# Kernel tuning notes

Hardware: AMD Instinct MI355X
Metric: run time of the kernel (lower is better)

The kernel has to match this reference:

```python
import jax, jax.numpy as jnp
import numpy as np

B, S, D, H = 2, 2048, 1024, 16
DK = D // H


def setup_inputs() -> dict:
    key = jax.random.key(0)
    ks = jax.random.split(key, 9)
    def xavier(k, shape):
        fan_in, fan_out = shape[1], shape[0]
        lim = jnp.sqrt(6.0 / (fan_in + fan_out))
        return jax.random.uniform(k, shape, jnp.float32, -lim, lim)
    x = jax.random.normal(ks[0], (B, S, D), jnp.float32)
    mask = jnp.ones((B, 1, S), jnp.int32)
    Wq = xavier(ks[1], (D, D)); bq = jnp.zeros((D,), jnp.float32)
    Wk = xavier(ks[2], (D, D)); bk = jnp.zeros((D,), jnp.float32)
    Wv = xavier(ks[3], (D, D)); bv = jnp.zeros((D,), jnp.float32)
    Wo = xavier(ks[4], (D, D)); bo = jnp.zeros((D,), jnp.float32)
    return {"x": x, "mask": mask, "Wq": Wq, "bq": bq, "Wk": Wk, "bk": bk,
            "Wv": Wv, "bv": bv, "Wo": Wo, "bo": bo}


def reference(x, mask, Wq, bq, Wk, bk, Wv, bv, Wo, bo):
    # Linear layers use torch convention y = x @ W.T + b
    q = (x @ Wq.T + bq).reshape(B, S, H, DK).transpose(0, 2, 1, 3)  # [B,H,S,DK]
    k = (x @ Wk.T + bk).reshape(B, S, H, DK).transpose(0, 2, 1, 3)
    v = (x @ Wv.T + bv).reshape(B, S, H, DK).transpose(0, 2, 1, 3)
    scores = jnp.einsum('bhqd,bhkd->bhqk', q, k) / jnp.sqrt(jnp.float32(DK))
    m = mask[:, None, :, :]  # unsqueeze(1): broadcast over heads -> [B,1,1,S]
    scores = jnp.where(m == 0, jnp.float32(-1e9), scores)
    p = jax.nn.softmax(scores, axis=-1)  # dropout p=0.0 -> identity
    ctx = jnp.einsum('bhqk,bhkd->bhqd', p, v)
    ctx = ctx.transpose(0, 2, 1, 3).reshape(B, S, D)
    return ctx @ Wo.T + bo
```

## Files before the change

### kernel.cpp

```cpp
#include <hip/hip_runtime.h>
#include <hip/hip_bf16.h>
#include <math.h>

#define Bn 2
#define Sn 2048
#define Dn 1024
#define Hn 16
#define DKn 64
#define BHS (Bn * Hn * Sn)

using fragb  = __attribute__((ext_vector_type(8))) short;
using frag16 = __attribute__((ext_vector_type(8))) _Float16;
using f4     = __attribute__((ext_vector_type(4))) float;

__device__ __forceinline__ short f2bf(float f) {
    union { float f; unsigned u; } v; v.f = f;
    unsigned r = v.u + 0x7FFF + ((v.u >> 16) & 1);
    return (short)(r >> 16);
}
__device__ __forceinline__ short f2h(float f) {
    _Float16 h = (_Float16)f;
    short s; __builtin_memcpy(&s, &h, 2); return s;
}

#define GLOAD(gptr, lptr)                                                     \
    __builtin_amdgcn_global_load_lds(                                         \
        (const __attribute__((address_space(1))) unsigned int*)(const void*)(gptr), \
        (__attribute__((address_space(3))) unsigned int*)(void*)(lptr), 16, 0, 0)

#define NX (Bn * Sn * Dn)
#define NW (Dn * Dn)

__global__ __launch_bounds__(256) void prep(
    const float* __restrict__ x,  const float* __restrict__ Wq,
    const float* __restrict__ Wk, const float* __restrict__ Wv,
    const float* __restrict__ Wo, const int* __restrict__ mask,
    short* __restrict__ xh,
    short* __restrict__ Wqh, short* __restrict__ Wkh,
    short* __restrict__ Wvh, short* __restrict__ Woh,
    short* __restrict__ mfb)
{
    int i = blockIdx.x * 256 + threadIdx.x;
    const float* src; short* dst; int j;
    if (i < NX)               { src = x;  dst = xh;  j = i; }
    else if (i < NX + NW)     { src = Wq; dst = Wqh; j = i - NX; }
    else if (i < NX + 2 * NW) { src = Wk; dst = Wkh; j = i - NX - NW; }
    else if (i < NX + 3 * NW) { src = Wv; dst = Wvh; j = i - NX - 2 * NW; }
    else if (i < NX + 4 * NW) { src = Wo; dst = Woh; j = i - NX - 3 * NW; }
    else {
        j = i - NX - 4 * NW;
        if (j < Bn * Sn) mfb[j] = mask[j] ? (short)0x3F80 : (short)0;
        return;
    }
    dst[j] = f2h(src[j]);
}

#define BN 128
#define BK 64

template <int BMT>
__global__ __launch_bounds__(256) void gemm_mfma(
    const short* __restrict__ A,
    const short* __restrict__ W0, const float* __restrict__ b0,
    const short* __restrict__ W1, const float* __restrict__ b1,
    const short* __restrict__ W2, const float* __restrict__ b2,
    const int* __restrict__ mask,
    short* __restrict__ Qb, short* __restrict__ Kb, short* __restrict__ Vtb,
    float* __restrict__ outf, int mode)
{
    constexpr int MI = BMT / 32;
    __shared__ __align__(16) short As[BMT * BK];
    __shared__ __align__(16) short Bs[BN * BK];

    const int tid  = threadIdx.x;
    const int wave = tid >> 6;
    const int lane = tid & 63;
    const int quad = lane >> 4;
    const int l16  = lane & 15;
    const int wm   = wave >> 1;
    const int wn   = wave & 1;

    const int m0   = blockIdx.y * BMT;
    const int n0   = blockIdx.x * BN;
    const int widx = n0 >> 10;
    const int nl0  = n0 & 1023;

    const short* Wp   = widx == 0 ? W0 : (widx == 1 ? W1 : W2);
    const float* bias = widx == 0 ? b0 : (widx == 1 ? b1 : b2);

    f4 acc[MI][4];
    #pragma unroll
    for (int i = 0; i < MI; i++)
        #pragma unroll
        for (int j = 0; j < 4; j++) {
            acc[i][j][0] = 0.f; acc[i][j][1] = 0.f;
            acc[i][j][2] = 0.f; acc[i][j][3] = 0.f;
        }

    const int K = Dn;
    const int lr = lane >> 3;
    const int sc = ((lane & 7) ^ lr) * 8;
    const short* Apl = A  + (size_t)(m0  + lr) * K + sc;
    const short* Bpl = Wp + (size_t)(nl0 + lr) * K + sc;

    const int ca0 = ((quad ^ (l16 & 7)) * 8);
    const int ca1 = (((quad + 4) ^ (l16 & 7)) * 8);

    for (int k0 = 0; k0 < K; k0 += BK) {
        __syncthreads();
        if constexpr (BMT == 128) {
            #pragma unroll
            for (int g = 0; g < 4; g++)
                GLOAD(Apl + (size_t)(wave * 32 + g * 8) * K + k0,
                      &As[(wave * 32 + g * 8) * BK]);
        } else {
            #pragma unroll
            for (int g = 0; g < 2; g++)
                GLOAD(Apl + (size_t)(wave * 16 + g * 8) * K + k0,
                      &As[(wave * 16 + g * 8) * BK]);
        }
        #pragma unroll
        for (int g = 0; g < 4; g++)
            GLOAD(Bpl + (size_t)(wave * 32 + g * 8) * K + k0,
                  &Bs[(wave * 32 + g * 8) * BK]);
        __syncthreads();

        #pragma unroll
        for (int ki = 0; ki < 2; ki++) {
            const int ca = ki ? ca1 : ca0;
            frag16 a[MI], b[4];
            #pragma unroll
            for (int mi = 0; mi < MI; mi++)
                a[mi] = *(const frag16*)&As[(wm * (BMT / 2) + mi * 16 + l16) * BK + ca];
            #pragma unroll
            for (int ni = 0; ni < 4; ni++)
                b[ni] = *(const frag16*)&Bs[(wn * 64 + ni * 16 + l16) * BK + ca];
            #pragma unroll
            for (int mi = 0; mi < MI; mi++)
                #pragma unroll
                for (int ni = 0; ni < 4; ni++)
                    acc[mi][ni] = __builtin_amdgcn_mfma_f32_16x16x32_f16(
                        a[mi], b[ni], acc[mi][ni], 0, 0, 0);
        }
    }

    const float QSCALE = 0.125f * 1.44269504088896340736f;

    #pragma unroll
    for (int mi = 0; mi < MI; mi++) {
        #pragma unroll
        for (int ni = 0; ni < 4; ni++) {
            int nl = nl0 + wn * 64 + ni * 16 + l16;
            float bv = bias[nl];
            #pragma unroll
            for (int r = 0; r < 4; r++) {
                int m = m0 + wm * (BMT / 2) + mi * 16 + quad * 4 + r;
                float v = acc[mi][ni][r] + bv;
                if (mode == 0) {
                    int b  = m >> 11, s = m & (Sn - 1);
                    int h  = nl >> 6, dk = nl & 63;
                    if (widx == 0)
                        Qb[((size_t)(b * Hn + h) * Sn + s) * DKn + dk] = f2bf(v * QSCALE);
                    else if (widx == 1)
                        Kb[((size_t)(b * Hn + h) * Sn + s) * DKn + dk] = f2bf(v);
                    else {
                        float mv = (float)mask[b * Sn + s];
                        Vtb[((size_t)(b * Hn + h) * DKn + dk) * Sn + s] = f2bf(v * mv);
                    }
                } else {
                    outf[(size_t)m * Dn + nl] = v;
                }
            }
        }
    }
}

#define LP  72

__global__ __launch_bounds__(256) void attn_mfma(
    const short* __restrict__ Qb, const short* __restrict__ Kb,
    const short* __restrict__ Vtb, const short* __restrict__ mfb,
    float* __restrict__ ctxp0, float* __restrict__ ctxp1,
    float* __restrict__ lp)
{
    __shared__ __align__(16) short Ks[64 * 64];
    __shared__ __align__(16) short Vs[64 * 64];
    __shared__ short Ps[4][32 * LP];
    __shared__ __align__(16) short mfs[64];

    const int tid  = threadIdx.x;
    const int wave = tid >> 6;
    const int lane = tid & 63;
    const int quad = lane >> 4;
    const int l16  = lane & 15;

    const int split = blockIdx.x & 1;
    const int rest  = blockIdx.x >> 1;
    const int qt  = rest & 15;
    const int bhh = rest >> 4;
    const int b   = bhh >> 4;
    const int h   = bhh & 15;

    fragb qf[2][2];
    #pragma unroll
    for (int w = 0; w < 2; w++) {
        int qrow = qt * 128 + wave * 32 + w * 16 + l16;
        const short* qptr = Qb + ((size_t)bhh * Sn + qrow) * DKn + quad * 8;
        qf[w][0] = *(const fragb*)(qptr);
        qf[w][1] = *(const fragb*)(qptr + 32);
    }

    f4 ctx[2][4];
    #pragma unroll
    for (int w = 0; w < 2; w++)
        #pragma unroll
        for (int dt = 0; dt < 4; dt++) {
            ctx[w][dt][0] = 0.f; ctx[w][dt][1] = 0.f;
            ctx[w][dt][2] = 0.f; ctx[w][dt][3] = 0.f;
        }
    f4 lacc[2];
    lacc[0][0] = 0.f; lacc[0][1] = 0.f; lacc[0][2] = 0.f; lacc[0][3] = 0.f;
    lacc[1] = lacc[0];

    const int lr = lane >> 3;
    const int sc = ((lane & 7) ^ lr) * 8;
    const short* Kg = Kb  + (size_t)bhh * Sn * DKn;
    const short* Vg = Vtb + (size_t)bhh * DKn * Sn;
    const short* mg = mfb + (size_t)b * Sn;

    const short* Ksrc = Kg + (size_t)(wave * 16 + lr) * DKn + sc;
    const short* Vsrc = Vg + (size_t)(wave * 16 + lr) * Sn + sc;

    const int c0 = ((quad ^ (l16 & 7)) * 8);

    const int kt0 = split * 16;
    for (int kt = kt0; kt < kt0 + 16; kt++) {
        __syncthreads();
        GLOAD(Ksrc + (size_t)kt * 4096,             &Ks[(wave * 16) * 64]);
        GLOAD(Ksrc + (size_t)kt * 4096 + 8 * DKn,   &Ks[(wave * 16 + 8) * 64]);
        GLOAD(Vsrc + (size_t)kt * 64,               &Vs[(wave * 16) * 64]);
        GLOAD(Vsrc + (size_t)kt * 64 + 8 * Sn,      &Vs[(wave * 16 + 8) * 64]);
        if (tid < 8)
            *(uint4*)&mfs[tid * 8] = *(const uint4*)(mg + kt * 64 + tid * 8);
        __syncthreads();

        #pragma unroll
        for (int t = 0; t < 4; t++) {
            fragb k0 = *(const fragb*)&Ks[(t * 16 + l16) * 64 + c0];
            fragb k1 = *(const fragb*)&Ks[(t * 16 + l16) * 64 + (c0 ^ 32)];
            #pragma unroll
            for (int w = 0; w < 2; w++) {
                f4 a; a[0] = 0.f; a[1] = 0.f; a[2] = 0.f; a[3] = 0.f;
                a = __builtin_amdgcn_mfma_f32_16x16x32_bf16(k0, qf[w][0], a, 0, 0, 0);
                a = __builtin_amdgcn_mfma_f32_16x16x32_bf16(k1, qf[w][1], a, 0, 0, 0);
                unsigned u0 = __float_as_uint(exp2f(a[0]));
                unsigned u1 = __float_as_uint(exp2f(a[1]));
                unsigned u2 = __float_as_uint(exp2f(a[2]));
                unsigned u3 = __float_as_uint(exp2f(a[3]));
                uint2 pw;
                pw.x = __builtin_amdgcn_perm(u1, u0, 0x07060302u);
                pw.y = __builtin_amdgcn_perm(u3, u2, 0x07060302u);
                *(uint2*)&Ps[wave][(w * 16 + l16) * LP + 16 * t + quad * 4] = pw;
            }
        }

        fragb p[2][2];
        #pragma unroll
        for (int w = 0; w < 2; w++) {
            p[w][0] = *(const fragb*)&Ps[wave][(w * 16 + l16) * LP + quad * 8];
            p[w][1] = *(const fragb*)&Ps[wave][(w * 16 + l16) * LP + quad * 8 + 32];
        }
        fragb m0 = *(const fragb*)&mfs[quad * 8];
        fragb m1 = *(const fragb*)&mfs[quad * 8 + 32];
        #pragma unroll
        for (int w = 0; w < 2; w++) {
            lacc[w] = __builtin_amdgcn_mfma_f32_16x16x32_bf16(p[w][0], m0, lacc[w], 0, 0, 0);
            lacc[w] = __builtin_amdgcn_mfma_f32_16x16x32_bf16(p[w][1], m1, lacc[w], 0, 0, 0);
        }
        #pragma unroll
        for (int dt = 0; dt < 4; dt++) {
            fragb v0 = *(const fragb*)&Vs[(dt * 16 + l16) * 64 + c0];
            fragb v1 = *(const fragb*)&Vs[(dt * 16 + l16) * 64 + (c0 ^ 32)];
            #pragma unroll
            for (int w = 0; w < 2; w++) {
                ctx[w][dt] = __builtin_amdgcn_mfma_f32_16x16x32_bf16(p[w][0], v0, ctx[w][dt], 0, 0, 0);
                ctx[w][dt] = __builtin_amdgcn_mfma_f32_16x16x32_bf16(p[w][1], v1, ctx[w][dt], 0, 0, 0);
            }
        }
    }

    float* cp  = split ? ctxp1 : ctxp0;
    float* lpp = lp + (size_t)split * BHS;
    #pragma unroll
    for (int w = 0; w < 2; w++)
        #pragma unroll
        for (int r = 0; r < 4; r++) {
            int row = qt * 128 + wave * 32 + w * 16 + quad * 4 + r;
            if (l16 == 0) lpp[(size_t)bhh * Sn + row] = lacc[w][r];
            #pragma unroll
            for (int dt = 0; dt < 4; dt++)
                cp[((size_t)(b * Sn + row)) * Dn + h * DKn + dt * 16 + l16] =
                    ctx[w][dt][r];
        }
}

__global__ __launch_bounds__(256) void reduce_ctx(
    const float* __restrict__ c0, const float* __restrict__ c1,
    const float* __restrict__ lp, short* __restrict__ Ch)
{
    int i4 = blockIdx.x * 256 + threadIdx.x;
    int e    = i4 << 2;
    int brow = e >> 10;
    int d    = e & 1023;
    int b    = brow >> 11;
    int row  = brow & (Sn - 1);
    int h    = d >> 6;
    size_t li = (size_t)(b * Hn + h) * Sn + row;
    float l = lp[li] + lp[BHS + li];
    float inv = 1.f / l;
    float4 v0 = ((const float4*)c0)[i4];
    float4 v1 = ((const float4*)c1)[i4];
    ushort4 o;
    o.x = (unsigned short)f2h((v0.x + v1.x) * inv);
    o.y = (unsigned short)f2h((v0.y + v1.y) * inv);
    o.z = (unsigned short)f2h((v0.z + v1.z) * inv);
    o.w = (unsigned short)f2h((v0.w + v1.w) * inv);
    ((ushort4*)Ch)[i4] = o;
}

extern "C" void kernel_launch(void* const* d_in, const int* in_sizes, int n_in,
                              void* d_out, int out_size, void* d_ws, size_t ws_size,
                              hipStream_t stream) {
    const float* x    = (const float*)d_in[0];
    const int*   mask = (const int*)d_in[1];
    const float* Wq   = (const float*)d_in[2];
    const float* bq   = (const float*)d_in[3];
    const float* Wk   = (const float*)d_in[4];
    const float* bk   = (const float*)d_in[5];
    const float* Wv   = (const float*)d_in[6];
    const float* bv   = (const float*)d_in[7];
    const float* Wo   = (const float*)d_in[8];
    const float* bo   = (const float*)d_in[9];
    float* out = (float*)d_out;

    char* ws = (char*)d_ws;
    const size_t MB = 1024u * 1024u;
    short* xh    = (short*)(ws + 0 * MB);
    short* Wqh   = (short*)(ws + 8 * MB);
    short* Wkh   = (short*)(ws + 10 * MB);
    short* Wvh   = (short*)(ws + 12 * MB);
    short* Qb    = (short*)(ws + 16 * MB);
    short* Kb    = (short*)(ws + 24 * MB);
    short* Vtb   = (short*)(ws + 32 * MB);
    float* ctxp0 = (float*)(ws + 0 * MB);
    float* ctxp1 = (float*)(ws + 40 * MB);
    short* Woh   = (short*)(ws + 56 * MB);
    float* lp    = (float*)(ws + 58 * MB);
    short* mfb   = (short*)(ws + 59 * MB);
    short* Ch    = (short*)(ws + 60 * MB);

    const int TOT = NX + 4 * NW + Bn * Sn;
    prep<<<(TOT + 255) / 256, 256, 0, stream>>>(
        x, Wq, Wk, Wv, Wo, mask, xh, Wqh, Wkh, Wvh, Woh, mfb);

    gemm_mfma<128><<<dim3(24, 32), 256, 0, stream>>>(
        xh, Wqh, bq, Wkh, bk, Wvh, bv, mask,
        Qb, Kb, Vtb, nullptr, 0);

    attn_mfma<<<dim3(Bn * Hn * (Sn / 128) * 2), 256, 0, stream>>>(
        Qb, Kb, Vtb, mfb, ctxp0, ctxp1, lp);

    reduce_ctx<<<dim3(NX / 4 / 256), 256, 0, stream>>>(ctxp0, ctxp1, lp, Ch);

    gemm_mfma<64><<<dim3(8, 64), 256, 0, stream>>>(
        Ch, Woh, bo, Woh, bo, Woh, bo, mask,
        nullptr, nullptr, nullptr, out, 1);
}
```

Measured before the change: 225.6 us.

## Vectorize prep conversion and split GEMM into QKV and output kernels with BK=32

```diff
diff --git a/kernel.cpp b/kernel.cpp
--- a/kernel.cpp
+++ b/kernel.cpp
@@ -18,9 +18,9 @@
     unsigned r = v.u + 0x7FFF + ((v.u >> 16) & 1);
     return (short)(r >> 16);
 }
-__device__ __forceinline__ short f2h(float f) {
+__device__ __forceinline__ unsigned short f2h(float f) {
     _Float16 h = (_Float16)f;
-    short s; __builtin_memcpy(&s, &h, 2); return s;
+    unsigned short s; __builtin_memcpy(&s, &h, 2); return s;
 }
 
 #define GLOAD(gptr, lptr)                                                     \
@@ -30,6 +30,7 @@
 
 #define NX (Bn * Sn * Dn)
 #define NW (Dn * Dn)
+#define NF4 ((NX + 4 * NW) / 4)
 
 __global__ __launch_bounds__(256) void prep(
     const float* __restrict__ x,  const float* __restrict__ Wq,
@@ -41,36 +42,40 @@
     short* __restrict__ mfb)
 {
     int i = blockIdx.x * 256 + threadIdx.x;
-    const float* src; short* dst; int j;
-    if (i < NX)               { src = x;  dst = xh;  j = i; }
-    else if (i < NX + NW)     { src = Wq; dst = Wqh; j = i - NX; }
-    else if (i < NX + 2 * NW) { src = Wk; dst = Wkh; j = i - NX - NW; }
-    else if (i < NX + 3 * NW) { src = Wv; dst = Wvh; j = i - NX - 2 * NW; }
-    else if (i < NX + 4 * NW) { src = Wo; dst = Woh; j = i - NX - 3 * NW; }
-    else {
-        j = i - NX - 4 * NW;
-        if (j < Bn * Sn) mfb[j] = mask[j] ? (short)0x3F80 : (short)0;
-        return;
-    }
-    dst[j] = f2h(src[j]);
-}
-
-#define BN 128
-#define BK 64
-
-template <int BMT>
-__global__ __launch_bounds__(256) void gemm_mfma(
+    if (i < NF4) {
+        int e = i << 2;
+        const float* src; short* dst; int j;
+        if (e < NX)               { src = x;  dst = xh;  j = e; }
+        else if (e < NX + NW)     { src = Wq; dst = Wqh; j = e - NX; }
+        else if (e < NX + 2 * NW) { src = Wk; dst = Wkh; j = e - NX - NW; }
+        else if (e < NX + 3 * NW) { src = Wv; dst = Wvh; j = e - NX - 2 * NW; }
+        else                      { src = Wo; dst = Woh; j = e - NX - 3 * NW; }
+        float4 v = *(const float4*)(src + j);
+        ushort4 o;
+        o.x = f2h(v.x); o.y = f2h(v.y); o.z = f2h(v.z); o.w = f2h(v.w);
+        *(ushort4*)(dst + j) = o;
+    } else {
+        int j = (i - NF4) << 2;
+        if (j < Bn * Sn) {
+            int4 m = *(const int4*)(mask + j);
+            ushort4 o;
+            o.x = m.x ? 0x3F80 : 0; o.y = m.y ? 0x3F80 : 0;
+            o.z = m.z ? 0x3F80 : 0; o.w = m.w ? 0x3F80 : 0;
+            *(ushort4*)(mfb + j) = o;
+        }
+    }
+}
+
+__global__ __launch_bounds__(256) void gemm_qkv(
     const short* __restrict__ A,
     const short* __restrict__ W0, const float* __restrict__ b0,
     const short* __restrict__ W1, const float* __restrict__ b1,
     const short* __restrict__ W2, const float* __restrict__ b2,
     const int* __restrict__ mask,
-    short* __restrict__ Qb, short* __restrict__ Kb, short* __restrict__ Vtb,
-    float* __restrict__ outf, int mode)
+    short* __restrict__ Qb, short* __restrict__ Kb, short* __restrict__ Vtb)
 {
-    constexpr int MI = BMT / 32;
-    __shared__ __align__(16) short As[BMT * BK];
-    __shared__ __align__(16) short Bs[BN * BK];
+    __shared__ __align__(16) short As[128 * 32];
+    __shared__ __align__(16) short Bs[128 * 32];
 
     const int tid  = threadIdx.x;
     const int wave = tid >> 6;
@@ -80,17 +85,17 @@
     const int wm   = wave >> 1;
     const int wn   = wave & 1;
 
-    const int m0   = blockIdx.y * BMT;
-    const int n0   = blockIdx.x * BN;
+    const int m0   = blockIdx.y * 128;
+    const int n0   = blockIdx.x * 128;
     const int widx = n0 >> 10;
     const int nl0  = n0 & 1023;
 
     const short* Wp   = widx == 0 ? W0 : (widx == 1 ? W1 : W2);
     const float* bias = widx == 0 ? b0 : (widx == 1 ? b1 : b2);
 
-    f4 acc[MI][4];
-    #pragma unroll
-    for (int i = 0; i < MI; i++)
+    f4 acc[4][4];
+    #pragma unroll
+    for (int i = 0; i < 4; i++)
         #pragma unroll
         for (int j = 0; j < 4; j++) {
             acc[i][j][0] = 0.f; acc[i][j][1] = 0.f;
@@ -98,78 +103,129 @@
         }
 
     const int K = Dn;
-    const int lr = lane >> 3;
-    const int sc = ((lane & 7) ^ lr) * 8;
-    const short* Apl = A  + (size_t)(m0  + lr) * K + sc;
-    const short* Bpl = Wp + (size_t)(nl0 + lr) * K + sc;
-
-    const int ca0 = ((quad ^ (l16 & 7)) * 8);
-    const int ca1 = (((quad + 4) ^ (l16 & 7)) * 8);
-
-    for (int k0 = 0; k0 < K; k0 += BK) {
-        __syncthreads();
-        if constexpr (BMT == 128) {
-            #pragma unroll
-            for (int g = 0; g < 4; g++)
-                GLOAD(Apl + (size_t)(wave * 32 + g * 8) * K + k0,
-                      &As[(wave * 32 + g * 8) * BK]);
-        } else {
-            #pragma unroll
-            for (int g = 0; g < 2; g++)
-                GLOAD(Apl + (size_t)(wave * 16 + g * 8) * K + k0,
-                      &As[(wave * 16 + g * 8) * BK]);
-        }
-        #pragma unroll
-        for (int g = 0; g < 4; g++)
-            GLOAD(Bpl + (size_t)(wave * 32 + g * 8) * K + k0,
-                  &Bs[(wave * 32 + g * 8) * BK]);
-        __syncthreads();
-
-        #pragma unroll
-        for (int ki = 0; ki < 2; ki++) {
-            const int ca = ki ? ca1 : ca0;
-            frag16 a[MI], b[4];
-            #pragma unroll
-            for (int mi = 0; mi < MI; mi++)
-                a[mi] = *(const frag16*)&As[(wm * (BMT / 2) + mi * 16 + l16) * BK + ca];
+    const int r0  = tid >> 2,         kc0 = (tid & 3) * 8;
+    const int r1  = (tid + 256) >> 2;
+    const short* Ar0 = A  + (size_t)(m0 + r0) * K + kc0;
+    const short* Ar1 = A  + (size_t)(m0 + r1) * K + kc0;
+    const short* Br0 = Wp + (size_t)(nl0 + r0) * K + kc0;
+    const short* Br1 = Wp + (size_t)(nl0 + r1) * K + kc0;
+
+    for (int k0 = 0; k0 < K; k0 += 32) {
+        __syncthreads();
+        GLOAD(Ar0 + k0, &As[(wave * 64) * 8]);
+        GLOAD(Ar1 + k0, &As[(256 + wave * 64) * 8]);
+        GLOAD(Br0 + k0, &Bs[(wave * 64) * 8]);
+        GLOAD(Br1 + k0, &Bs[(256 + wave * 64) * 8]);
+        __syncthreads();
+
+        frag16 a[4], b[4];
+        #pragma unroll
+        for (int mi = 0; mi < 4; mi++)
+            a[mi] = *(const frag16*)&As[(wm * 64 + mi * 16 + l16) * 32 + quad * 8];
+        #pragma unroll
+        for (int ni = 0; ni < 4; ni++)
+            b[ni] = *(const frag16*)&Bs[(wn * 64 + ni * 16 + l16) * 32 + quad * 8];
+        #pragma unroll
+        for (int mi = 0; mi < 4; mi++)
             #pragma unroll
             for (int ni = 0; ni < 4; ni++)
-                b[ni] = *(const frag16*)&Bs[(wn * 64 + ni * 16 + l16) * BK + ca];
-            #pragma unroll
-            for (int mi = 0; mi < MI; mi++)
-                #pragma unroll
-                for (int ni = 0; ni < 4; ni++)
-                    acc[mi][ni] = __builtin_amdgcn_mfma_f32_16x16x32_f16(
-                        a[mi], b[ni], acc[mi][ni], 0, 0, 0);
-        }
+                acc[mi][ni] = __builtin_amdgcn_mfma_f32_16x16x32_f16(
+                    a[mi], b[ni], acc[mi][ni], 0, 0, 0);
     }
 
     const float QSCALE = 0.125f * 1.44269504088896340736f;
 
     #pragma unroll
-    for (int mi = 0; mi < MI; mi++) {
+    for (int mi = 0; mi < 4; mi++) {
         #pragma unroll
         for (int ni = 0; ni < 4; ni++) {
             int nl = nl0 + wn * 64 + ni * 16 + l16;
             float bv = bias[nl];
             #pragma unroll
             for (int r = 0; r < 4; r++) {
-                int m = m0 + wm * (BMT / 2) + mi * 16 + quad * 4 + r;
+                int m = m0 + wm * 64 + mi * 16 + quad * 4 + r;
                 float v = acc[mi][ni][r] + bv;
-                if (mode == 0) {
-                    int b  = m >> 11, s = m & (Sn - 1);
-                    int h  = nl >> 6, dk = nl & 63;
-                    if (widx == 0)
-                        Qb[((size_t)(b * Hn + h) * Sn + s) * DKn + dk] = f2bf(v * QSCALE);
-                    else if (widx == 1)
-                        Kb[((size_t)(b * Hn + h) * Sn + s) * DKn + dk] = f2bf(v);
-                    else {
-                        float mv = (float)mask[b * Sn + s];
-                        Vtb[((size_t)(b * Hn + h) * DKn + dk) * Sn + s] = f2bf(v * mv);
-                    }
-                } else {
-                    outf[(size_t)m * Dn + nl] = v;
+                int b  = m >> 11, s = m & (Sn - 1);
+                int h  = nl >> 6, dk = nl & 63;
+                if (widx == 0)
+                    Qb[((size_t)(b * Hn + h) * Sn + s) * DKn + dk] = f2bf(v * QSCALE);
+                else if (widx == 1)
+                    Kb[((size_t)(b * Hn + h) * Sn + s) * DKn + dk] = f2bf(v);
+                else {
+                    float mv = (float)mask[b * Sn + s];
+                    Vtb[((size_t)(b * Hn + h) * DKn + dk) * Sn + s] = f2bf(v * mv);
                 }
+            }
+        }
+    }
+}
+
+__global__ __launch_bounds__(256) void gemm_out(
+    const short* __restrict__ A, const short* __restrict__ Wp,
+    const float* __restrict__ bias, float* __restrict__ outf)
+{
+    __shared__ __align__(16) short As[64 * 32];
+    __shared__ __align__(16) short Bs[128 * 32];
+
+    const int tid  = threadIdx.x;
+    const int wave = tid >> 6;
+    const int lane = tid & 63;
+    const int quad = lane >> 4;
+    const int l16  = lane & 15;
+    const int wm   = wave >> 1;
+    const int wn   = wave & 1;
+
+    const int m0 = blockIdx.y * 64;
+    const int n0 = blockIdx.x * 128;
+
+    f4 acc[2][4];
+    #pragma unroll
+    for (int i = 0; i < 2; i++)
+        #pragma unroll
+        for (int j = 0; j < 4; j++) {
+            acc[i][j][0] = 0.f; acc[i][j][1] = 0.f;
+            acc[i][j][2] = 0.f; acc[i][j][3] = 0.f;
+        }
+
+    const int K = Dn;
+    const int r0  = tid >> 2,         kc0 = (tid & 3) * 8;
+    const int r1  = (tid + 256) >> 2;
+    const short* Ar0 = A  + (size_t)(m0 + r0) * K + kc0;
+    const short* Br0 = Wp + (size_t)(n0 + r0) * K + kc0;
+    const short* Br1 = Wp + (size_t)(n0 + r1) * K + kc0;
+
+    for (int k0 = 0; k0 < K; k0 += 32) {
+        __syncthreads();
+        GLOAD(Ar0 + k0, &As[(wave * 64) * 8]);
+        GLOAD(Br0 + k0, &Bs[(wave * 64) * 8]);
+        GLOAD(Br1 + k0, &Bs[(256 + wave * 64) * 8]);
+        __syncthreads();
+
+        frag16 a[2], b[4];
+        #pragma unroll
+        for (int mi = 0; mi < 2; mi++)
+            a[mi] = *(const frag16*)&As[(wm * 32 + mi * 16 + l16) * 32 + quad * 8];
+        #pragma unroll
+        for (int ni = 0; ni < 4; ni++)
+            b[ni] = *(const frag16*)&Bs[(wn * 64 + ni * 16 + l16) * 32 + quad * 8];
+        #pragma unroll
+        for (int mi = 0; mi < 2; mi++)
+            #pragma unroll
+            for (int ni = 0; ni < 4; ni++)
+                acc[mi][ni] = __builtin_amdgcn_mfma_f32_16x16x32_f16(
+                    a[mi], b[ni], acc[mi][ni], 0, 0, 0);
+    }
+
+    #pragma unroll
+    for (int mi = 0; mi < 2; mi++) {
+        #pragma unroll
+        for (int ni = 0; ni < 4; ni++) {
+            int nl = n0 + wn * 64 + ni * 16 + l16;
+            float bv = bias[nl];
+            #pragma unroll
+            for (int r = 0; r < 4; r++) {
+                int m = m0 + wm * 32 + mi * 16 + quad * 4 + r;
+                outf[(size_t)m * Dn + nl] = acc[mi][ni][r] + bv;
             }
         }
     }
@@ -321,10 +377,10 @@
     float4 v0 = ((const float4*)c0)[i4];
     float4 v1 = ((const float4*)c1)[i4];
     ushort4 o;
-    o.x = (unsigned short)f2h((v0.x + v1.x) * inv);
-    o.y = (unsigned short)f2h((v0.y + v1.y) * inv);
-    o.z = (unsigned short)f2h((v0.z + v1.z) * inv);
-    o.w = (unsigned short)f2h((v0.w + v1.w) * inv);
+    o.x = f2h((v0.x + v1.x) * inv);
+    o.y = f2h((v0.y + v1.y) * inv);
+    o.z = f2h((v0.z + v1.z) * inv);
+    o.w = f2h((v0.w + v1.w) * inv);
     ((ushort4*)Ch)[i4] = o;
 }
 
@@ -359,20 +415,17 @@
     short* mfb   = (short*)(ws + 59 * MB);
     short* Ch    = (short*)(ws + 60 * MB);
 
-    const int TOT = NX + 4 * NW + Bn * Sn;
-    prep<<<(TOT + 255) / 256, 256, 0, stream>>>(
+    const int PRE = NF4 + (Bn * Sn) / 4;
+    prep<<<(PRE + 255) / 256, 256, 0, stream>>>(
         x, Wq, Wk, Wv, Wo, mask, xh, Wqh, Wkh, Wvh, Woh, mfb);
 
-    gemm_mfma<128><<<dim3(24, 32), 256, 0, stream>>>(
-        xh, Wqh, bq, Wkh, bk, Wvh, bv, mask,
-        Qb, Kb, Vtb, nullptr, 0);
+    gemm_qkv<<<dim3(24, 32), 256, 0, stream>>>(
+        xh, Wqh, bq, Wkh, bk, Wvh, bv, mask, Qb, Kb, Vtb);
 
     attn_mfma<<<dim3(Bn * Hn * (Sn / 128) * 2), 256, 0, stream>>>(
         Qb, Kb, Vtb, mfb, ctxp0, ctxp1, lp);
 
     reduce_ctx<<<dim3(NX / 4 / 256), 256, 0, stream>>>(ctxp0, ctxp1, lp, Ch);
 
-    gemm_mfma<64><<<dim3(8, 64), 256, 0, stream>>>(
-        Ch, Woh, bo, Woh, bo, Woh, bo, mask,
-        nullptr, nullptr, nullptr, out, 1);
-}
+    gemm_out<<<dim3(8, 64), 256, 0, stream>>>(Ch, Woh, bo, out);
+}
```

Measured after the change: 223.7 us. Within noise of the previous version (-0.9%).
